# Kernel tuning notes

Measured on AMD Instinct MI355X. Metric: run time of the kernel, lower is better.

The kernel has to match this reference:

```python
import jax, jax.numpy as jnp
import numpy as np

B, L, H, C = 32, 2048, 512, 50
KERNEL = 3  # avgpool kernel, stride 1, pad 1, count_include_pad=False


def _avgpool3_no_pad_count(x):
    """AvgPool1d(kernel=3, stride=1, pad=1, count_include_pad=False) along last axis.
    x: (..., L). Zero-pad, sum 3-tap windows, divide by number of valid elements."""
    pad = [(0, 0)] * (x.ndim - 1) + [(1, 1)]
    xp = jnp.pad(x, pad)
    s = xp[..., :-2] + xp[..., 1:-1] + xp[..., 2:]
    ones = jnp.pad(jnp.ones_like(x), pad)
    cnt = ones[..., :-2] + ones[..., 1:-1] + ones[..., 2:]
    return s / cnt


def setup_inputs() -> dict:
    key = jax.random.key(0)
    k1, k2, k3, k4, k5, k6 = jax.random.split(key, 6)
    sent_keys = jax.random.normal(k1, (B, L, H), dtype=jnp.float32)
    sent_values = jax.random.normal(k2, (B, L, H), dtype=jnp.float32)
    sent_lens = jax.random.randint(k3, (B,), 1, L + 1).astype(jnp.int64)
    W1 = jax.random.normal(k4, (H, H), dtype=jnp.float32) * 0.02
    W2 = jax.random.normal(k5, (H, H), dtype=jnp.float32) * 0.02
    W3 = jax.random.normal(k6, (C, H), dtype=jnp.float32) * 0.02
    return {"sent_keys": sent_keys, "sent_values": sent_values,
            "sent_lens": sent_lens, "W1": W1, "W2": W2, "W3": W3}


def reference(sent_keys, sent_values, sent_lens, W1, W2, W3):
    # Tiny MLP scorer (dropout is identity in eval mode)
    p1 = jnp.tanh(jnp.einsum('blh,kh->blk', sent_keys, W1))   # (B,L,H)
    p2 = jnp.tanh(jnp.einsum('blh,kh->blk', p1, W2))          # (B,L,H)
    p3 = jnp.einsum('blh,ch->blc', p1 + p2, W3)               # (B,L,C)

    b, l, c = p3.shape
    # Fill padded positions with the score at the last valid position (index len-1)
    last_idx = (sent_lens - 1).astype(jnp.int32)[:, None, None]        # (B,1,1)
    last = jnp.take_along_axis(p3, jnp.broadcast_to(last_idx, (b, 1, c)), axis=1)  # (B,1,C)
    mask = (jnp.arange(l)[None, :] < sent_lens[:, None])[:, :, None]   # (B,L,1)
    kq = jnp.where(mask, p3, last)

    # Smooth along doc-position axis with avgpool(count_include_pad=False)
    smoothened_kq = _avgpool3_no_pad_count(kq.transpose(0, 2, 1)).transpose(0, 2, 1)  # (B,L,C)

    # Softmax over classes, then zero out padded positions
    attention_values = jax.nn.softmax(smoothened_kq, axis=2)
    attention_values = jnp.where(mask, attention_values, 0.0)

    # (B,C,L) @ (B,L,H) -> (B,C,H)
    class_inputs = jnp.einsum('blc,blh->bch', attention_values, sent_values)
    return attention_values, class_inputs, smoothened_kq
```

## Files before the change

kernel.cpp:

```cpp
#include <hip/hip_runtime.h>
#include <cstdint>

#define Bc 32
#define Lc 2048
#define Hc 512
#define Cc 50
#define PCc 52
#define Mc (Bc*Lc)

typedef short s8v   __attribute__((ext_vector_type(8)));
typedef float f4v   __attribute__((ext_vector_type(4)));

__device__ inline unsigned short f2bf(float f) {
    unsigned int u = __float_as_uint(f);
    u += 0x7fffu + ((u >> 16) & 1u);
    return (unsigned short)(u >> 16);
}
__device__ inline float bf2f(unsigned short h) {
    return __uint_as_float(((unsigned int)h) << 16);
}
__device__ inline float fast_tanh(float x) {
    float e = __expf(2.0f * x);
    return 1.0f - 2.0f / (e + 1.0f);
}
__device__ inline void gl_lds16(const unsigned short* g, unsigned short* l) {
    __builtin_amdgcn_global_load_lds(
        (const __attribute__((address_space(1))) unsigned int*)g,
        (__attribute__((address_space(3))) unsigned int*)l, 16, 0, 0);
}

__global__ __launch_bounds__(256)
void f32_to_bf16_kernel(const float* __restrict__ in, unsigned short* __restrict__ out)
{
    size_t i = ((size_t)blockIdx.x * 256 + threadIdx.x) * 8;
    float4 a = *(const float4*)(in + i);
    float4 b = *(const float4*)(in + i + 4);
    s8v o;
    o[0]=f2bf(a.x); o[1]=f2bf(a.y); o[2]=f2bf(a.z); o[3]=f2bf(a.w);
    o[4]=f2bf(b.x); o[5]=f2bf(b.y); o[6]=f2bf(b.z); o[7]=f2bf(b.w);
    *(s8v*)(out + i) = o;
}

__global__ __launch_bounds__(256)
void convert_weights_kernel(const float* __restrict__ W1, const float* __restrict__ W2,
                            const float* __restrict__ W3,
                            unsigned short* __restrict__ W1b,
                            unsigned short* __restrict__ W2b,
                            unsigned short* __restrict__ W3b)
{
    int e = (blockIdx.x * 256 + threadIdx.x) * 8;
    if (e >= 524288) {
        int off = e - 524288;
        int row = off >> 9;
        s8v o;
        #pragma unroll
        for (int j = 0; j < 8; ++j)
            o[j] = (row < Cc) ? (short)f2bf(W3[off + j]) : (short)0;
        *(s8v*)(W3b + off) = o;
        return;
    }
    const float* src = (e < 262144) ? W1 : W2;
    unsigned short* dst = (e < 262144) ? W1b : W2b;
    int off = (e < 262144) ? e : e - 262144;
    float4 a = *(const float4*)(src + off);
    float4 b = *(const float4*)(src + off + 4);
    s8v o;
    o[0]=f2bf(a.x); o[1]=f2bf(a.y); o[2]=f2bf(a.z); o[3]=f2bf(a.w);
    o[4]=f2bf(b.x); o[5]=f2bf(b.y); o[6]=f2bf(b.z); o[7]=f2bf(b.w);
    *(s8v*)(dst + off) = o;
}

__global__ __launch_bounds__(256)
void transpose_v_kernel(const float* __restrict__ V, unsigned short* __restrict__ Vt)
{
    __shared__ float tile[64 * 65];
    const int l0 = blockIdx.x * 64;
    const int h0 = blockIdx.y * 64;
    const int b  = blockIdx.z;
    const int tid = threadIdx.x;
    const int li = tid >> 2;
    const int hq = (tid & 3) * 4;

    const float* src = V + ((size_t)(b * Lc + l0 + li)) * Hc + h0 + hq;
    #pragma unroll
    for (int j = 0; j < 4; ++j) {
        float4 v = *(const float4*)(src + 16 * j);
        float* d = &tile[li * 65 + hq + 16 * j];
        d[0] = v.x; d[1] = v.y; d[2] = v.z; d[3] = v.w;
    }
    __syncthreads();

    const int lane = tid & 63;
    const int w    = tid >> 6;
    #pragma unroll
    for (int i = 0; i < 16; ++i) {
        int hr = i * 4 + w;
        unsigned short* dst = Vt + ((size_t)(b * Hc + h0 + hr)) * Lc + l0 + lane;
        *dst = f2bf(tile[lane * 65 + hr]);
    }
}

__global__ __launch_bounds__(256)
void mfma_gemm512(const unsigned short* __restrict__ Ab,
                  const unsigned short* __restrict__ Wb,
                  unsigned short* __restrict__ Ob, int mode)
{
    __shared__ alignas(16) unsigned short As[128 * 32];
    __shared__ alignas(16) unsigned short Bs[128 * 32];
    __shared__ alignas(16) float Esf[32 * 133];
    const int tid = threadIdx.x;
    const int w = tid >> 6, l = tid & 63;

    const int bid = blockIdx.x;
    const int ixd = bid >> 3;
    const int y   = (bid & 7) * 64 + (ixd >> 2);
    const int x   = ixd & 3;
    const int j0 = x * 128;
    const int i0 = y * 128;

    const int sr  = w * 16 + (l >> 2);
    const int kg8 = (l & 3) * 8;
    const unsigned short* Ag0 = Ab + (size_t)(i0 + sr) * 512 + kg8;
    const unsigned short* Ag1 = Ag0 + (size_t)64 * 512;
    const unsigned short* Bg0 = Wb + (size_t)(j0 + sr) * 512 + kg8;
    const unsigned short* Bg1 = Bg0 + (size_t)64 * 512;
    unsigned short* Al0 = As + w * 512;
    unsigned short* Al1 = As + 2048 + w * 512;
    unsigned short* Bl0 = Bs + w * 512;
    unsigned short* Bl1 = Bs + 2048 + w * 512;

    const int wm = (w & 1) * 64, wn = (w >> 1) * 64;
    const int fr = l & 15;
    const int fq = (l >> 4) * 8;

    f4v acc[4][4];
    #pragma unroll
    for (int r = 0; r < 4; ++r)
        #pragma unroll
        for (int c = 0; c < 4; ++c) acc[r][c] = (f4v){0.f, 0.f, 0.f, 0.f};

    for (int k0 = 0; k0 < 512; k0 += 32) {
        gl_lds16(Ag0 + k0, Al0);
        gl_lds16(Ag1 + k0, Al1);
        gl_lds16(Bg0 + k0, Bl0);
        gl_lds16(Bg1 + k0, Bl1);
        __syncthreads();
        s8v af[4], bf[4];
        #pragma unroll
        for (int r = 0; r < 4; ++r)
            af[r] = *(const s8v*)&As[(wm + r * 16 + fr) * 32 + fq];
        #pragma unroll
        for (int c = 0; c < 4; ++c)
            bf[c] = *(const s8v*)&Bs[(wn + c * 16 + fr) * 32 + fq];
        #pragma unroll
        for (int r = 0; r < 4; ++r)
            #pragma unroll
            for (int c = 0; c < 4; ++c)
                acc[r][c] = __builtin_amdgcn_mfma_f32_16x16x32_bf16(
                    af[r], bf[c], acc[r][c], 0, 0, 0);
        __syncthreads();
    }

    #pragma unroll
    for (int h = 0; h < 4; ++h) {
        if (h) __syncthreads();
        if ((w & 1) == (h >> 1)) {
            const int rr = (h & 1) * 2;
            #pragma unroll
            for (int r = 0; r < 2; ++r)
                #pragma unroll
                for (int c = 0; c < 4; ++c)
                    #pragma unroll
                    for (int v = 0; v < 4; ++v) {
                        int row = r * 16 + (l >> 4) * 4 + v;
                        int col = wn + c * 16 + fr;
                        Esf[row * 133 + col] = fast_tanh(acc[rr + r][c][v]);
                    }
        }
        __syncthreads();
        #pragma unroll
        for (int t = 0; t < 4; ++t) {
            int chunk = t * 256 + tid;
            int row = chunk >> 5;
            int c4  = (chunk & 31) * 4;
            f4v val = *(const f4v*)&Esf[row * 133 + c4];
            size_t gr   = (size_t)(i0 + (h >> 1) * 64 + (h & 1) * 32 + row);
            size_t goff = gr * 512 + j0 + c4;
            ushort4 o;
            if (mode) {
                ushort4 a = *(const ushort4*)(Ab + goff);
                o.x = f2bf(val[0] + bf2f(a.x));
                o.y = f2bf(val[1] + bf2f(a.y));
                o.z = f2bf(val[2] + bf2f(a.z));
                o.w = f2bf(val[3] + bf2f(a.w));
            } else {
                o.x = f2bf(val[0]); o.y = f2bf(val[1]);
                o.z = f2bf(val[2]); o.w = f2bf(val[3]);
            }
            *(ushort4*)(Ob + goff) = o;
        }
    }
}

__global__ __launch_bounds__(256)
void mfma_gemm_p3(const unsigned short* __restrict__ Sb,
                  const unsigned short* __restrict__ W3b,
                  float* __restrict__ P3)
{
    __shared__ alignas(16) unsigned short As[128 * 32];
    __shared__ alignas(16) unsigned short Bs[64 * 32];
    const int tid = threadIdx.x;
    const int w = tid >> 6, l = tid & 63;
    const int i0 = blockIdx.x * 128;

    const int sr  = w * 16 + (l >> 2);
    const int kg8 = (l & 3) * 8;
    const unsigned short* Ag0 = Sb + (size_t)(i0 + sr) * 512 + kg8;
    const unsigned short* Ag1 = Ag0 + (size_t)64 * 512;
    const unsigned short* Bg  = W3b + (size_t)sr * 512 + kg8;
    unsigned short* Al0 = As + w * 512;
    unsigned short* Al1 = As + 2048 + w * 512;
    unsigned short* Bl  = Bs + w * 512;

    const int wm = w * 32;
    const int fr = l & 15;
    const int fq = (l >> 4) * 8;

    f4v acc[2][4];
    #pragma unroll
    for (int r = 0; r < 2; ++r)
        #pragma unroll
        for (int c = 0; c < 4; ++c) acc[r][c] = (f4v){0.f, 0.f, 0.f, 0.f};

    for (int k0 = 0; k0 < 512; k0 += 32) {
        gl_lds16(Ag0 + k0, Al0);
        gl_lds16(Ag1 + k0, Al1);
        gl_lds16(Bg + k0, Bl);
        __syncthreads();
        s8v af[2], bf[4];
        #pragma unroll
        for (int r = 0; r < 2; ++r)
            af[r] = *(const s8v*)&As[(wm + r * 16 + fr) * 32 + fq];
        #pragma unroll
        for (int c = 0; c < 4; ++c)
            bf[c] = *(const s8v*)&Bs[(c * 16 + fr) * 32 + fq];
        #pragma unroll
        for (int r = 0; r < 2; ++r)
            #pragma unroll
            for (int c = 0; c < 4; ++c)
                acc[r][c] = __builtin_amdgcn_mfma_f32_16x16x32_bf16(
                    af[r], bf[c], acc[r][c], 0, 0, 0);
        __syncthreads();
    }

    #pragma unroll
    for (int r = 0; r < 2; ++r)
        #pragma unroll
        for (int v = 0; v < 4; ++v) {
            const int row = i0 + wm + r * 16 + (l >> 4) * 4 + v;
            #pragma unroll
            for (int c = 0; c < 4; ++c) {
                const int col = c * 16 + fr;
                if (col < Cc) P3[(size_t)row * PCc + col] = acc[r][c][v];
            }
        }
}

__global__ __launch_bounds__(64)
void normalize_lens_kernel(const int* __restrict__ raw, int* __restrict__ lens)
{
    __shared__ int is64;
    if (threadIdx.x == 0) {
        int orv = 0;
        for (int i = 1; i < 32; i += 2) orv |= raw[i];
        is64 = (orv == 0) ? 1 : 0;
    }
    __syncthreads();
    int b = threadIdx.x;
    if (b < Bc) lens[b] = is64 ? raw[2*b] : raw[b];
}

__global__ __launch_bounds__(256)
void pool_softmax_kernel(const float* __restrict__ P3, const int* __restrict__ lens,
                         float* __restrict__ out_attn, float* __restrict__ out_smooth,
                         unsigned short* __restrict__ attnT)
{
    const int idx = blockIdx.x * 256 + threadIdx.x;
    const int b = idx >> 11;
    const int l = idx & (Lc - 1);
    const int len = lens[b];
    const float* base = P3 + (size_t)b * Lc * PCc;

    const int  r0 = min(l, len - 1);
    const bool hm = (l > 0);
    const bool hp = (l < Lc - 1);
    const int  rm = hm ? min(l - 1, len - 1) : 0;
    const int  rp = hp ? min(l + 1, len - 1) : 0;
    const float rcnt = 1.f / (1.f + (hm ? 1.f : 0.f) + (hp ? 1.f : 0.f));

    float sm[PCc];
    const float* p0 = base + (size_t)r0 * PCc;
    #pragma unroll
    for (int q = 0; q < 13; ++q) {
        f4v v = *(const f4v*)(p0 + q * 4);
        sm[q*4+0] = v[0]; sm[q*4+1] = v[1]; sm[q*4+2] = v[2]; sm[q*4+3] = v[3];
    }
    if (hm) {
        const float* p = base + (size_t)rm * PCc;
        #pragma unroll
        for (int q = 0; q < 13; ++q) {
            f4v v = *(const f4v*)(p + q * 4);
            sm[q*4+0] += v[0]; sm[q*4+1] += v[1]; sm[q*4+2] += v[2]; sm[q*4+3] += v[3];
        }
    }
    if (hp) {
        const float* p = base + (size_t)rp * PCc;
        #pragma unroll
        for (int q = 0; q < 13; ++q) {
            f4v v = *(const f4v*)(p + q * 4);
            sm[q*4+0] += v[0]; sm[q*4+1] += v[1]; sm[q*4+2] += v[2]; sm[q*4+3] += v[3];
        }
    }

    float mx = -1e30f;
    #pragma unroll
    for (int c = 0; c < Cc; ++c) {
        sm[c] *= rcnt;
        mx = fmaxf(mx, sm[c]);
    }
    float* srow = out_smooth + (size_t)idx * Cc;
    #pragma unroll
    for (int q = 0; q < 25; ++q) {
        float2 v = make_float2(sm[q*2], sm[q*2+1]);
        *(float2*)(srow + q * 2) = v;
    }

    float sum = 0.f;
    #pragma unroll
    for (int c = 0; c < Cc; ++c) {
        float e = __expf(sm[c] - mx);
        sm[c] = e;
        sum += e;
    }
    const float inv = 1.f / sum;
    const bool valid = (l < len);
    const float scale = valid ? inv : 0.f;
    float* arow = out_attn + (size_t)idx * Cc;
    unsigned short* trow = attnT + (size_t)b * 64 * Lc + l;
    #pragma unroll
    for (int c = 0; c < Cc; ++c) sm[c] *= scale;
    #pragma unroll
    for (int q = 0; q < 25; ++q)
        *(float2*)(arow + q * 2) = make_float2(sm[q*2], sm[q*2+1]);
    #pragma unroll
    for (int c = 0; c < Cc; ++c)
        trow[(size_t)c * Lc] = f2bf(sm[c]);
}

__global__ __launch_bounds__(256)
void class_mfma_kernel(const unsigned short* __restrict__ attnT,
                       const unsigned short* __restrict__ Vt,
                       float* __restrict__ out_class)
{
    __shared__ alignas(16) unsigned short As[64 * 32];
    __shared__ alignas(16) unsigned short Bs[128 * 32];
    const int tid = threadIdx.x;
    const int w = tid >> 6, l = tid & 63;
    const int n0 = blockIdx.x * 128;
    const int b  = blockIdx.y;
    const int kb = blockIdx.z * 512;

    const int sr  = w * 16 + (l >> 2);
    const int kg8 = (l & 3) * 8;
    const unsigned short* Ag  = attnT + ((size_t)b * 64 + sr) * Lc + kg8;
    const unsigned short* Bg0 = Vt + ((size_t)(b * Hc + n0 + sr)) * Lc + kg8;
    const unsigned short* Bg1 = Bg0 + (size_t)64 * Lc;
    unsigned short* Al  = As + w * 512;
    unsigned short* Bl0 = Bs + w * 512;
    unsigned short* Bl1 = Bs + 2048 + w * 512;

    const int fr = l & 15;
    const int fq = (l >> 4) * 8;

    f4v acc[4][2];
    #pragma unroll
    for (int r = 0; r < 4; ++r)
        #pragma unroll
        for (int c = 0; c < 2; ++c) acc[r][c] = (f4v){0.f, 0.f, 0.f, 0.f};

    for (int k0 = kb; k0 < kb + 512; k0 += 32) {
        gl_lds16(Ag + k0, Al);
        gl_lds16(Bg0 + k0, Bl0);
        gl_lds16(Bg1 + k0, Bl1);
        __syncthreads();
        s8v af[4], bf[2];
        #pragma unroll
        for (int r = 0; r < 4; ++r)
            af[r] = *(const s8v*)&As[(r * 16 + fr) * 32 + fq];
        #pragma unroll
        for (int c = 0; c < 2; ++c)
            bf[c] = *(const s8v*)&Bs[(w * 32 + c * 16 + fr) * 32 + fq];
        #pragma unroll
        for (int r = 0; r < 4; ++r)
            #pragma unroll
            for (int c = 0; c < 2; ++c)
                acc[r][c] = __builtin_amdgcn_mfma_f32_16x16x32_bf16(
                    af[r], bf[c], acc[r][c], 0, 0, 0);
        __syncthreads();
    }

    #pragma unroll
    for (int r = 0; r < 4; ++r)
        #pragma unroll
        for (int v = 0; v < 4; ++v) {
            const int m = r * 16 + (l >> 4) * 4 + v;
            if (m < Cc) {
                #pragma unroll
                for (int c = 0; c < 2; ++c) {
                    const int h = n0 + w * 32 + c * 16 + fr;
                    atomicAdd(out_class + ((size_t)b * Cc + m) * Hc + h,
                              acc[r][c][v]);
                }
            }
        }
}

extern "C" void kernel_launch(void* const* d_in, const int* in_sizes, int n_in,
                              void* d_out, int out_size, void* d_ws, size_t ws_size,
                              hipStream_t stream)
{
    const float* keys     = (const float*)d_in[0];
    const float* vals     = (const float*)d_in[1];
    const int*   lens_raw = (const int*)d_in[2];
    const float* W1       = (const float*)d_in[3];
    const float* W2       = (const float*)d_in[4];
    const float* W3       = (const float*)d_in[5];

    char* ws = (char*)d_ws;
    const size_t MB = 1024 * 1024;
    unsigned short* Akv  = (unsigned short*)ws;
    float*          P3   = (float*)ws;
    unsigned short* P1b  = (unsigned short*)(ws + 64 * MB);
    unsigned short* Vt   = (unsigned short*)(ws + 64 * MB);
    unsigned short* Sb   = (unsigned short*)(ws + 128 * MB);
    unsigned short* W1b  = (unsigned short*)(ws + 192 * MB);
    unsigned short* W2b  = W1b + Hc * Hc;
    unsigned short* W3b  = W2b + Hc * Hc;
    unsigned short* attnT= (unsigned short*)(ws + 194 * MB);
    int*            lens = (int*)(ws + 202 * MB);

    float* out_attn   = (float*)d_out;
    float* out_class  = out_attn + (size_t)Bc * Lc * Cc;
    float* out_smooth = out_class + (size_t)Bc * Cc * Hc;

    hipMemsetAsync(out_class, 0, (size_t)Bc * Cc * Hc * sizeof(float), stream);

    f32_to_bf16_kernel<<<(Mc * Hc / 8) / 256, 256, 0, stream>>>(keys, Akv);
    convert_weights_kernel<<<272, 256, 0, stream>>>(W1, W2, W3, W1b, W2b, W3b);
    normalize_lens_kernel<<<1, 64, 0, stream>>>(lens_raw, lens);

    mfma_gemm512<<<2048, 256, 0, stream>>>(Akv, W1b, P1b, 0);
    mfma_gemm512<<<2048, 256, 0, stream>>>(P1b, W2b, Sb, 1);
    transpose_v_kernel<<<dim3(Lc / 64, Hc / 64, Bc), 256, 0, stream>>>(vals, Vt);
    mfma_gemm_p3<<<Mc / 128, 256, 0, stream>>>(Sb, W3b, P3);
    pool_softmax_kernel<<<Mc / 256, 256, 0, stream>>>(P3, lens, out_attn, out_smooth, attnT);
    class_mfma_kernel<<<dim3(4, Bc, 4), 256, 0, stream>>>(attnT, Vt, out_class);
}
```

Baseline: 499.0 us.

## Fuse W3 projection into second GEMM epilogue with atomic accumulation; vectorize Vt stores

The second 512x512 GEMM now keeps its tanh+residual output tile in shared memory and directly multiplies it by the matching 128-column slice of W3. Partial class scores are accumulated into P3 with float atomics after a memset, which removes the S intermediate buffer write/read and the separate p3 GEMM launch. The V transpose kernel now writes four bf16 values per store instead of scalar stores. The costs are four-way atomic contention per P3 element, a non-deterministic summation order, W3 fragments read directly from global memory, and higher LDS use per block, which may reduce occupancy.

Result: slower. 544.0 us (+9.0%).

```diff
diff --git a/kernel.cpp b/kernel.cpp
--- a/kernel.cpp
+++ b/kernel.cpp
@@ -91,19 +91,24 @@
     __syncthreads();
 
     const int lane = tid & 63;
-    const int w    = tid >> 6;
-    #pragma unroll
-    for (int i = 0; i < 16; ++i) {
-        int hr = i * 4 + w;
-        unsigned short* dst = Vt + ((size_t)(b * Hc + h0 + hr)) * Lc + l0 + lane;
-        *dst = f2bf(tile[lane * 65 + hr]);
+    const int w4   = tid >> 6;
+    const int lpos = (lane & 15) * 4;
+    #pragma unroll
+    for (int i = 0; i < 4; ++i) {
+        int hr = i * 16 + w4 * 4 + (lane >> 4);
+        ushort4 o;
+        o.x = f2bf(tile[(lpos + 0) * 65 + hr]);
+        o.y = f2bf(tile[(lpos + 1) * 65 + hr]);
+        o.z = f2bf(tile[(lpos + 2) * 65 + hr]);
+        o.w = f2bf(tile[(lpos + 3) * 65 + hr]);
+        *(ushort4*)(Vt + ((size_t)(b * Hc + h0 + hr)) * Lc + l0 + lpos) = o;
     }
 }
 
 __global__ __launch_bounds__(256)
 void mfma_gemm512(const unsigned short* __restrict__ Ab,
                   const unsigned short* __restrict__ Wb,
-                  unsigned short* __restrict__ Ob, int mode)
+                  unsigned short* __restrict__ Ob)
 {
     __shared__ alignas(16) unsigned short As[128 * 32];
     __shared__ alignas(16) unsigned short Bs[128 * 32];
@@ -187,65 +192,71 @@
             size_t gr   = (size_t)(i0 + (h >> 1) * 64 + (h & 1) * 32 + row);
             size_t goff = gr * 512 + j0 + c4;
             ushort4 o;
-            if (mode) {
-                ushort4 a = *(const ushort4*)(Ab + goff);
-                o.x = f2bf(val[0] + bf2f(a.x));
-                o.y = f2bf(val[1] + bf2f(a.y));
-                o.z = f2bf(val[2] + bf2f(a.z));
-                o.w = f2bf(val[3] + bf2f(a.w));
-            } else {
-                o.x = f2bf(val[0]); o.y = f2bf(val[1]);
-                o.z = f2bf(val[2]); o.w = f2bf(val[3]);
-            }
+            o.x = f2bf(val[0]); o.y = f2bf(val[1]);
+            o.z = f2bf(val[2]); o.w = f2bf(val[3]);
             *(ushort4*)(Ob + goff) = o;
         }
     }
 }
 
 __global__ __launch_bounds__(256)
-void mfma_gemm_p3(const unsigned short* __restrict__ Sb,
-                  const unsigned short* __restrict__ W3b,
-                  float* __restrict__ P3)
-{
-    __shared__ alignas(16) unsigned short As[128 * 32];
-    __shared__ alignas(16) unsigned short Bs[64 * 32];
+void mfma_gemm512_fused(const unsigned short* __restrict__ Ab,
+                        const unsigned short* __restrict__ Wb,
+                        const unsigned short* __restrict__ W3g,
+                        float* __restrict__ P3)
+{
+    __shared__ alignas(16) char smem[51840];
+    unsigned short* As  = (unsigned short*)smem;
+    unsigned short* Bs  = (unsigned short*)(smem + 8192);
+    float*          Esf = (float*)smem;
+    unsigned short* Ss  = (unsigned short*)(smem + 17024);
+
     const int tid = threadIdx.x;
     const int w = tid >> 6, l = tid & 63;
-    const int i0 = blockIdx.x * 128;
+
+    const int bid = blockIdx.x;
+    const int ixd = bid >> 3;
+    const int y   = (bid & 7) * 64 + (ixd >> 2);
+    const int x   = ixd & 3;
+    const int j0 = x * 128;
+    const int i0 = y * 128;
 
     const int sr  = w * 16 + (l >> 2);
     const int kg8 = (l & 3) * 8;
-    const unsigned short* Ag0 = Sb + (size_t)(i0 + sr) * 512 + kg8;
+    const unsigned short* Ag0 = Ab + (size_t)(i0 + sr) * 512 + kg8;
     const unsigned short* Ag1 = Ag0 + (size_t)64 * 512;
-    const unsigned short* Bg  = W3b + (size_t)sr * 512 + kg8;
+    const unsigned short* Bg0 = Wb + (size_t)(j0 + sr) * 512 + kg8;
+    const unsigned short* Bg1 = Bg0 + (size_t)64 * 512;
     unsigned short* Al0 = As + w * 512;
     unsigned short* Al1 = As + 2048 + w * 512;
-    unsigned short* Bl  = Bs + w * 512;
-
-    const int wm = w * 32;
+    unsigned short* Bl0 = Bs + w * 512;
+    unsigned short* Bl1 = Bs + 2048 + w * 512;
+
+    const int wm = (w & 1) * 64, wn = (w >> 1) * 64;
     const int fr = l & 15;
     const int fq = (l >> 4) * 8;
 
-    f4v acc[2][4];
-    #pragma unroll
-    for (int r = 0; r < 2; ++r)
+    f4v acc[4][4];
+    #pragma unroll
+    for (int r = 0; r < 4; ++r)
         #pragma unroll
         for (int c = 0; c < 4; ++c) acc[r][c] = (f4v){0.f, 0.f, 0.f, 0.f};
 
     for (int k0 = 0; k0 < 512; k0 += 32) {
         gl_lds16(Ag0 + k0, Al0);
         gl_lds16(Ag1 + k0, Al1);
-        gl_lds16(Bg + k0, Bl);
-        __syncthreads();
-        s8v af[2], bf[4];
-        #pragma unroll
-        for (int r = 0; r < 2; ++r)
+        gl_lds16(Bg0 + k0, Bl0);
+        gl_lds16(Bg1 + k0, Bl1);
+        __syncthreads();
+        s8v af[4], bf[4];
+        #pragma unroll
+        for (int r = 0; r < 4; ++r)
             af[r] = *(const s8v*)&As[(wm + r * 16 + fr) * 32 + fq];
         #pragma unroll
         for (int c = 0; c < 4; ++c)
-            bf[c] = *(const s8v*)&Bs[(c * 16 + fr) * 32 + fq];
-        #pragma unroll
-        for (int r = 0; r < 2; ++r)
+            bf[c] = *(const s8v*)&Bs[(wn + c * 16 + fr) * 32 + fq];
+        #pragma unroll
+        for (int r = 0; r < 4; ++r)
             #pragma unroll
             for (int c = 0; c < 4; ++c)
                 acc[r][c] = __builtin_amdgcn_mfma_f32_16x16x32_bf16(
@@ -254,14 +265,74 @@
     }
 
     #pragma unroll
+    for (int h = 0; h < 4; ++h) {
+        if (h) __syncthreads();
+        if ((w & 1) == (h >> 1)) {
+            const int rr = (h & 1) * 2;
+            #pragma unroll
+            for (int r = 0; r < 2; ++r)
+                #pragma unroll
+                for (int c = 0; c < 4; ++c)
+                    #pragma unroll
+                    for (int v = 0; v < 4; ++v) {
+                        int row = r * 16 + (l >> 4) * 4 + v;
+                        int col = wn + c * 16 + fr;
+                        Esf[row * 133 + col] = fast_tanh(acc[rr + r][c][v]);
+                    }
+        }
+        __syncthreads();
+        #pragma unroll
+        for (int t = 0; t < 4; ++t) {
+            int chunk = t * 256 + tid;
+            int row = chunk >> 5;
+            int c4  = (chunk & 31) * 4;
+            f4v val = *(const f4v*)&Esf[row * 133 + c4];
+            const int lr = (h >> 1) * 64 + (h & 1) * 32 + row;
+            size_t goff = (size_t)(i0 + lr) * 512 + j0 + c4;
+            ushort4 a = *(const ushort4*)(Ab + goff);
+            ushort4 o;
+            o.x = f2bf(val[0] + bf2f(a.x));
+            o.y = f2bf(val[1] + bf2f(a.y));
+            o.z = f2bf(val[2] + bf2f(a.z));
+            o.w = f2bf(val[3] + bf2f(a.w));
+            *(ushort4*)&Ss[lr * 136 + c4] = o;
+        }
+    }
+    __syncthreads();
+
+    f4v acc3[2][4];
+    #pragma unroll
     for (int r = 0; r < 2; ++r)
         #pragma unroll
+        for (int c = 0; c < 4; ++c) acc3[r][c] = (f4v){0.f, 0.f, 0.f, 0.f};
+
+    #pragma unroll
+    for (int ks = 0; ks < 4; ++ks) {
+        s8v af3[2], bf3[4];
+        #pragma unroll
+        for (int r = 0; r < 2; ++r)
+            af3[r] = *(const s8v*)&Ss[(w * 32 + r * 16 + fr) * 136 + ks * 32 + fq];
+        #pragma unroll
+        for (int c = 0; c < 4; ++c)
+            bf3[c] = *(const s8v*)(W3g + (size_t)(c * 16 + fr) * 512 + j0 + ks * 32 + fq);
+        #pragma unroll
+        for (int r = 0; r < 2; ++r)
+            #pragma unroll
+            for (int c = 0; c < 4; ++c)
+                acc3[r][c] = __builtin_amdgcn_mfma_f32_16x16x32_bf16(
+                    af3[r], bf3[c], acc3[r][c], 0, 0, 0);
+    }
+
+    #pragma unroll
+    for (int r = 0; r < 2; ++r)
+        #pragma unroll
         for (int v = 0; v < 4; ++v) {
-            const int row = i0 + wm + r * 16 + (l >> 4) * 4 + v;
+            const int row = i0 + w * 32 + r * 16 + (l >> 4) * 4 + v;
             #pragma unroll
             for (int c = 0; c < 4; ++c) {
                 const int col = c * 16 + fr;
-                if (col < Cc) P3[(size_t)row * PCc + col] = acc[r][c][v];
+                if (col < Cc)
+                    atomicAdd(P3 + (size_t)row * PCc + col, acc3[r][c][v]);
             }
         }
 }
@@ -442,7 +513,6 @@
     float*          P3   = (float*)ws;
     unsigned short* P1b  = (unsigned short*)(ws + 64 * MB);
     unsigned short* Vt   = (unsigned short*)(ws + 64 * MB);
-    unsigned short* Sb   = (unsigned short*)(ws + 128 * MB);
     unsigned short* W1b  = (unsigned short*)(ws + 192 * MB);
     unsigned short* W2b  = W1b + Hc * Hc;
     unsigned short* W3b  = W2b + Hc * Hc;
@@ -459,10 +529,10 @@
     convert_weights_kernel<<<272, 256, 0, stream>>>(W1, W2, W3, W1b, W2b, W3b);
     normalize_lens_kernel<<<1, 64, 0, stream>>>(lens_raw, lens);
 
-    mfma_gemm512<<<2048, 256, 0, stream>>>(Akv, W1b, P1b, 0);
-    mfma_gemm512<<<2048, 256, 0, stream>>>(P1b, W2b, Sb, 1);
+    mfma_gemm512<<<2048, 256, 0, stream>>>(Akv, W1b, P1b);
+    hipMemsetAsync(P3, 0, (size_t)Bc * Lc * PCc * sizeof(float), stream);
+    mfma_gemm512_fused<<<2048, 256, 0, stream>>>(P1b, W2b, W3b, P3);
     transpose_v_kernel<<<dim3(Lc / 64, Hc / 64, Bc), 256, 0, stream>>>(vals, Vt);
-    mfma_gemm_p3<<<Mc / 128, 256, 0, stream>>>(Sb, W3b, P3);
     pool_softmax_kernel<<<Mc / 256, 256, 0, stream>>>(P3, lens, out_attn, out_smooth, attnT);
     class_mfma_kernel<<<dim3(4, Bc, 4), 256, 0, stream>>>(attnT, Vt, out_class);
 }
```
